# Optimization experiments

Measured on AMD Instinct MI355X. Metric: run time of the kernel, lower is better.

## Reference

```python
import jax, jax.numpy as jnp
import numpy as np

DN = jax.lax.conv_dimension_numbers((1, 32, 32, 32, 1), (3, 3, 3, 1, 32), ('NDHWC', 'DHWIO', 'NDHWC'))


def setup_inputs() -> dict:
    key = jax.random.key(0)
    k0, k1, k2, k3, k4 = jax.random.split(key, 5)
    B = 64
    x = jax.random.normal(k0, (B, 32, 32, 32, 1), dtype=jnp.float32)
    # conv weights in DHWIO layout; kaiming-ish scale
    w1 = jax.random.normal(k1, (3, 3, 3, 1, 32), dtype=jnp.float32) * (1.0 / np.sqrt(27 * 1))
    b1 = jax.random.normal(k2, (32,), dtype=jnp.float32) * 0.01
    w2 = jax.random.normal(k3, (3, 3, 3, 32, 64), dtype=jnp.float32) * (1.0 / np.sqrt(27 * 32))
    b2 = jax.random.normal(k4, (64,), dtype=jnp.float32) * 0.01
    return {"x": x, "w1": w1, "b1": b1, "w2": w2, "b2": b2}


def _conv3d_valid(x, w):
    # x: [B, D, H, W, C_in], w: [kD, kH, kW, C_in, C_out] -> [B, D-2, H-2, W-2, C_out]
    dn = jax.lax.conv_dimension_numbers(x.shape, w.shape, ('NDHWC', 'DHWIO', 'NDHWC'))
    return jax.lax.conv_general_dilated(x, w, window_strides=(1, 1, 1),
                                        padding='VALID', dimension_numbers=dn)


def reference(x, w1, b1, w2, b2):
    # Dense input -> all voxels active, so spconv's gather-GEMM-scatter equals
    # a dense valid 3D conv. ReLU acts on active-site features == dense ReLU.
    h = jax.nn.relu(_conv3d_valid(x, w1) + b1)        # [B, 30, 30, 30, 32]
    h = jax.nn.relu(_conv3d_valid(h, w2) + b2)        # [B, 28, 28, 28, 64]
    # spconv ToDense returns NCDHW
    return jnp.transpose(h, (0, 4, 1, 2, 3))          # [B, 64, 28, 28, 28]
```

## Files before the change

kernel.cpp:

```cpp
#include <hip/hip_runtime.h>
#include <cstdint>
#include <cstddef>

typedef __attribute__((ext_vector_type(8))) short bf16x8;
typedef __attribute__((ext_vector_type(4))) float f32x4;
typedef unsigned short u16;

#define H1_ROW_B   1920
#define H1_BATCH   (30 * 30 * 960)
#define LDS_STRIDE 1952
#define B_LDS_OFF  (36 * LDS_STRIDE)
#define OUT_CSTR   21952

__device__ __forceinline__ u16 f2bf(float f) {
    union { float f; unsigned u; } v; v.f = f;
    unsigned r = v.u + 0x7FFF + ((v.u >> 16) & 1);
    return (u16)(r >> 16);
}

__device__ __forceinline__ void fma4(float4& a, float s, const float4& w) {
    a.x = fmaf(s, w.x, a.x);
    a.y = fmaf(s, w.y, a.y);
    a.z = fmaf(s, w.z, a.z);
    a.w = fmaf(s, w.w, a.w);
}

__global__ __launch_bounds__(256) void conv1_relu(
    const float* __restrict__ x, const float* __restrict__ w1,
    const float* __restrict__ b1, u16* __restrict__ h1, int b0)
{
    __shared__ float wl[27 * 32 + 32];

    const int z   = blockIdx.x;
    const int yt  = blockIdx.y;
    const int bl  = blockIdx.z;
    const int b   = b0 + bl;
    const int tid = threadIdx.x;

    for (int i = tid; i < 27 * 32; i += 256) wl[i] = w1[i];
    if (tid < 32) wl[27 * 32 + tid] = b1[tid];
    __syncthreads();

    const int c4   = tid & 7;
    const int slot = tid >> 3;

    const float4 bias = *reinterpret_cast<const float4*>(&wl[27 * 32 + c4 * 4]);
    const float* xb  = x + (size_t)b * 32768;
    u16*         h1b = h1 + (size_t)bl * H1_BATCH;

    if (slot < 30) {
#pragma unroll 1
        for (int j = 0; j < 3; ++j) {
            const int p  = slot + 30 * j;
            const int yy = p / 15;
            const int xx = (p - yy * 15) * 2;
            const int y  = yt * 6 + yy;

            float4 acc0 = bias, acc1 = bias;
#pragma unroll
            for (int kd = 0; kd < 3; ++kd) {
#pragma unroll
                for (int kh = 0; kh < 3; ++kh) {
                    const float* row = xb + ((size_t)(z + kd) * 32 + (y + kh)) * 32 + xx;
                    const float2 v01 = *reinterpret_cast<const float2*>(row);
                    const float2 v23 = *reinterpret_cast<const float2*>(row + 2);
                    const int t = (kd * 3 + kh) * 3;
                    const float4 w0  = *reinterpret_cast<const float4*>(&wl[(t + 0) * 32 + c4 * 4]);
                    const float4 w1v = *reinterpret_cast<const float4*>(&wl[(t + 1) * 32 + c4 * 4]);
                    const float4 w2v = *reinterpret_cast<const float4*>(&wl[(t + 2) * 32 + c4 * 4]);
                    fma4(acc0, v01.x, w0);
                    fma4(acc0, v01.y, w1v);
                    fma4(acc0, v23.x, w2v);
                    fma4(acc1, v01.y, w0);
                    fma4(acc1, v23.x, w1v);
                    fma4(acc1, v23.y, w2v);
                }
            }
            ushort4 s0, s1;
            s0.x = f2bf(fmaxf(acc0.x, 0.f)); s0.y = f2bf(fmaxf(acc0.y, 0.f));
            s0.z = f2bf(fmaxf(acc0.z, 0.f)); s0.w = f2bf(fmaxf(acc0.w, 0.f));
            s1.x = f2bf(fmaxf(acc1.x, 0.f)); s1.y = f2bf(fmaxf(acc1.y, 0.f));
            s1.z = f2bf(fmaxf(acc1.z, 0.f)); s1.w = f2bf(fmaxf(acc1.w, 0.f));
            u16* dst = h1b + ((size_t)(z * 30 + y) * 30 + xx) * 32 + c4 * 4;
            *reinterpret_cast<ushort4*>(dst)      = s0;
            *reinterpret_cast<ushort4*>(dst + 32) = s1;
        }
    }
}

__global__ __launch_bounds__(256) void pack_w2(
    const float* __restrict__ w2, u16* __restrict__ wB)
{
    const int tap = blockIdx.x;
    const int tid = threadIdx.x;
    const int nt = tid >> 6;
    const int l  = tid & 63;
    const int r = l & 15, q = l >> 4;
    u16* dst = wB + ((size_t)(tap * 4 + nt) * 64 + l) * 8;
#pragma unroll
    for (int j = 0; j < 8; ++j)
        dst[j] = f2bf(w2[(size_t)(tap * 32 + q * 8 + j) * 64 + nt * 16 + r]);
}

template<int NMT, int XOUT>
__device__ __forceinline__ void conv2_body(
    const unsigned char* smem, const char* wBb,
    const float* __restrict__ b2, float* __restrict__ out,
    int b, int y0, int z0, int zw, int wv, int l)
{
    const int r = l & 15, q = l >> 4;
    const int yl = r >> 2, xg = r & 3;

    f32x4 acc[NMT][4];
#pragma unroll
    for (int nt = 0; nt < 4; ++nt) {
        const float bv = b2[nt * 16 + r];
        const f32x4 bi = {bv, bv, bv, bv};
#pragma unroll
        for (int mt = 0; mt < NMT; ++mt) acc[mt][nt] = bi;
    }

    const unsigned char* aBase =
        smem + (zw * 6 + yl) * LDS_STRIDE + (XOUT + xg) * 64 + q * 16;
    const unsigned char* bBase = smem + B_LDS_OFF + (size_t)l * 16;

#pragma unroll
    for (int tap = 0; tap < 27; ++tap) {
        if (tap < 26 && wv == ((tap + 1) & 7)) {
            const char* bsrc = wBb + (size_t)(tap + 1) * 4096 + l * 16;
            unsigned char* bdst = const_cast<unsigned char*>(
                smem) + B_LDS_OFF + ((tap + 1) & 1) * 4096 + l * 16;
#pragma unroll
            for (int k = 0; k < 4; ++k)
                __builtin_amdgcn_global_load_lds(
                    (const __attribute__((address_space(1))) void*)(bsrc + k * 1024),
                    (__attribute__((address_space(3))) void*)(bdst + k * 1024), 16, 0, 0);
        }

        const unsigned char* bb = bBase + (tap & 1) * 4096;
        const bf16x8 B0 = *reinterpret_cast<const bf16x8*>(bb);
        const bf16x8 B1 = *reinterpret_cast<const bf16x8*>(bb + 1024);
        const bf16x8 B2 = *reinterpret_cast<const bf16x8*>(bb + 2048);
        const bf16x8 B3 = *reinterpret_cast<const bf16x8*>(bb + 3072);

        const int kd = tap / 9;
        const int kh = (tap - kd * 9) / 3;
        const int kw = tap - kd * 9 - kh * 3;
        const unsigned char* ap = aBase + (kd * 6 + kh) * LDS_STRIDE + kw * 64;

        __builtin_amdgcn_s_setprio(1);
#pragma unroll
        for (int mt = 0; mt < NMT; ++mt) {
            const bf16x8 a = *reinterpret_cast<const bf16x8*>(ap + mt * 256);
            acc[mt][0] = __builtin_amdgcn_mfma_f32_16x16x32_bf16(a, B0, acc[mt][0], 0, 0, 0);
            acc[mt][1] = __builtin_amdgcn_mfma_f32_16x16x32_bf16(a, B1, acc[mt][1], 0, 0, 0);
            acc[mt][2] = __builtin_amdgcn_mfma_f32_16x16x32_bf16(a, B2, acc[mt][2], 0, 0, 0);
            acc[mt][3] = __builtin_amdgcn_mfma_f32_16x16x32_bf16(a, B3, acc[mt][3], 0, 0, 0);
        }
        __builtin_amdgcn_s_setprio(0);

        __syncthreads();
    }

    const int z = z0 + zw;
    float* ob = out + ((size_t)b * 64 + r) * OUT_CSTR
                    + (size_t)z * 784 + (size_t)(y0 + q) * 28 + XOUT;
#pragma unroll
    for (int mt = 0; mt < NMT; ++mt) {
#pragma unroll
        for (int nt = 0; nt < 4; ++nt) {
            const f32x4 v = acc[mt][nt];
            float4 st;
            st.x = fmaxf(v.x, 0.f);
            st.y = fmaxf(v.y, 0.f);
            st.z = fmaxf(v.z, 0.f);
            st.w = fmaxf(v.w, 0.f);
            *reinterpret_cast<float4*>(ob + (size_t)nt * 16 * OUT_CSTR + mt * 4) = st;
        }
    }
}

__global__ __launch_bounds__(512, 4) void conv2_mfma(
    const u16* __restrict__ h1, const u16* __restrict__ wB,
    const float* __restrict__ b2, float* __restrict__ out, int b0)
{
    __shared__ __align__(16) unsigned char smem[B_LDS_OFF + 8192];

    const int g   = gridDim.x;
    const int bid = blockIdx.x;
    const int lb  = (g % 8 == 0) ? ((bid & 7) * (g >> 3) + (bid >> 3)) : bid;

    const int t0  = lb % 49;
    const int bl  = lb / 49;
    const int yg  = t0 % 7;
    const int zt  = t0 / 7;

    const int b  = b0 + bl;
    const int y0 = yg * 4, z0 = zt * 4;
    const int tid = threadIdx.x;
    const int wv  = tid >> 6;
    const int l   = tid & 63;
    const int zw  = wv >> 1;
    const int xh  = wv & 1;

    const char* wBb = (const char*)wB;

    {
        const char* gbase = (const char*)(h1 + (size_t)bl * H1_BATCH);
        for (int c = wv; c < 72; c += 8) {
            const int rid = c >> 1, half = c & 1;
            const int zz = rid / 6, yy = rid - zz * 6;
            const char* src = gbase
                + (size_t)((z0 + zz) * 30 + (y0 + yy)) * H1_ROW_B
                + half * 896 + l * 16;
            unsigned char* dst = smem + rid * LDS_STRIDE + half * 896 + l * 16;
            __builtin_amdgcn_global_load_lds(
                (const __attribute__((address_space(1))) void*)src,
                (__attribute__((address_space(3))) void*)dst, 16, 0, 0);
        }
    }
    if (wv == 0) {
        const char* bsrc = wBb + l * 16;
        unsigned char* bdst = smem + B_LDS_OFF + l * 16;
#pragma unroll
        for (int k = 0; k < 4; ++k)
            __builtin_amdgcn_global_load_lds(
                (const __attribute__((address_space(1))) void*)(bsrc + k * 1024),
                (__attribute__((address_space(3))) void*)(bdst + k * 1024), 16, 0, 0);
    }
    __syncthreads();

    if (xh == 0)
        conv2_body<4, 0>(smem, wBb, b2, out, b, y0, z0, zw, wv, l);
    else
        conv2_body<3, 16>(smem, wBb, b2, out, b, y0, z0, zw, wv, l);
}

extern "C" void kernel_launch(void* const* d_in, const int* in_sizes, int n_in,
                              void* d_out, int out_size, void* d_ws, size_t ws_size,
                              hipStream_t stream)
{
    const float* x  = (const float*)d_in[0];
    const float* w1 = (const float*)d_in[1];
    const float* b1 = (const float*)d_in[2];
    const float* w2 = (const float*)d_in[3];
    const float* b2 = (const float*)d_in[4];
    float* out = (float*)d_out;

    u16* wB = (u16*)d_ws;
    u16* h1 = (u16*)((char*)d_ws + 131072);

    pack_w2<<<27, 256, 0, stream>>>(w2, wB);

    const size_t per_batch = (size_t)H1_BATCH * 2;
    size_t avail = ws_size > 131072 ? ws_size - 131072 : 0;
    int bchunk = (int)(avail / per_batch);
    if (bchunk < 1)  bchunk = 1;
    if (bchunk > 64) bchunk = 64;

    for (int b0 = 0; b0 < 64; b0 += bchunk) {
        int bc = 64 - b0;
        if (bc > bchunk) bc = bchunk;
        conv1_relu<<<dim3(30, 5, bc), 256, 0, stream>>>(x, w1, b1, h1, b0);
        conv2_mfma<<<dim3(49 * bc), 512, 0, stream>>>(h1, wB, b2, out, b0);
    }
}
```

Baseline: 304.3 us.

## Split conv2 tap loop into two MFMA halves with deeper weight prefetch

Reworks the conv2 inner loop so each tap's MFMAs are split into two halves around a raw s_barrier. The first half of the next tap's B fragments is read into registers early, and the global-to-LDS weight prefetch now runs two taps ahead instead of one. The goal is to hide LDS read and global load latency behind MFMA work and to drop the full __syncthreads, whose implicit waits stall every wave. It adds an extra barrier per tap, manual vmcnt waits and more register pressure, and any ordering mistake in the double buffer could cause a race.

```diff
diff --git a/kernel.cpp b/kernel.cpp
--- a/kernel.cpp
+++ b/kernel.cpp
@@ -23,6 +23,12 @@
     a.y = fmaf(s, w.y, a.y);
     a.z = fmaf(s, w.z, a.z);
     a.w = fmaf(s, w.w, a.w);
+}
+
+__device__ __forceinline__ void gld_lds(const char* src, unsigned char* dst) {
+    __builtin_amdgcn_global_load_lds(
+        (const __attribute__((address_space(1))) void*)src,
+        (__attribute__((address_space(3))) void*)dst, 16, 0, 0);
 }
 
 __global__ __launch_bounds__(256) void conv1_relu(
@@ -124,42 +130,65 @@
         smem + (zw * 6 + yl) * LDS_STRIDE + (XOUT + xg) * 64 + q * 16;
     const unsigned char* bBase = smem + B_LDS_OFF + (size_t)l * 16;
 
+    bf16x8 B01a = *reinterpret_cast<const bf16x8*>(bBase);
+    bf16x8 B01b = *reinterpret_cast<const bf16x8*>(bBase + 1024);
+    bf16x8 A_cur[NMT];
+    bf16x8 B23a, B23b;
+
 #pragma unroll
     for (int tap = 0; tap < 27; ++tap) {
-        if (tap < 26 && wv == ((tap + 1) & 7)) {
-            const char* bsrc = wBb + (size_t)(tap + 1) * 4096 + l * 16;
-            unsigned char* bdst = const_cast<unsigned char*>(
-                smem) + B_LDS_OFF + ((tap + 1) & 1) * 4096 + l * 16;
-#pragma unroll
-            for (int k = 0; k < 4; ++k)
-                __builtin_amdgcn_global_load_lds(
-                    (const __attribute__((address_space(1))) void*)(bsrc + k * 1024),
-                    (__attribute__((address_space(3))) void*)(bdst + k * 1024), 16, 0, 0);
-        }
-
-        const unsigned char* bb = bBase + (tap & 1) * 4096;
-        const bf16x8 B0 = *reinterpret_cast<const bf16x8*>(bb);
-        const bf16x8 B1 = *reinterpret_cast<const bf16x8*>(bb + 1024);
-        const bf16x8 B2 = *reinterpret_cast<const bf16x8*>(bb + 2048);
-        const bf16x8 B3 = *reinterpret_cast<const bf16x8*>(bb + 3072);
-
         const int kd = tap / 9;
         const int kh = (tap - kd * 9) / 3;
         const int kw = tap - kd * 9 - kh * 3;
         const unsigned char* ap = aBase + (kd * 6 + kh) * LDS_STRIDE + kw * 64;
+        const unsigned char* bb = bBase + (tap & 1) * 4096;
+
+#pragma unroll
+        for (int mt = 0; mt < NMT; ++mt)
+            A_cur[mt] = *reinterpret_cast<const bf16x8*>(ap + mt * 256);
+        B23a = *reinterpret_cast<const bf16x8*>(bb + 2048);
+        B23b = *reinterpret_cast<const bf16x8*>(bb + 3072);
 
         __builtin_amdgcn_s_setprio(1);
 #pragma unroll
         for (int mt = 0; mt < NMT; ++mt) {
-            const bf16x8 a = *reinterpret_cast<const bf16x8*>(ap + mt * 256);
-            acc[mt][0] = __builtin_amdgcn_mfma_f32_16x16x32_bf16(a, B0, acc[mt][0], 0, 0, 0);
-            acc[mt][1] = __builtin_amdgcn_mfma_f32_16x16x32_bf16(a, B1, acc[mt][1], 0, 0, 0);
-            acc[mt][2] = __builtin_amdgcn_mfma_f32_16x16x32_bf16(a, B2, acc[mt][2], 0, 0, 0);
-            acc[mt][3] = __builtin_amdgcn_mfma_f32_16x16x32_bf16(a, B3, acc[mt][3], 0, 0, 0);
+            acc[mt][0] = __builtin_amdgcn_mfma_f32_16x16x32_bf16(A_cur[mt], B01a, acc[mt][0], 0, 0, 0);
+            acc[mt][1] = __builtin_amdgcn_mfma_f32_16x16x32_bf16(A_cur[mt], B01b, acc[mt][1], 0, 0, 0);
         }
         __builtin_amdgcn_s_setprio(0);
 
-        __syncthreads();
+        if (tap < 26 && wv == ((tap + 1) & 7))
+            asm volatile("s_waitcnt vmcnt(0)");
+
+        __builtin_amdgcn_sched_barrier(0);
+        __builtin_amdgcn_s_barrier();
+        __builtin_amdgcn_sched_barrier(0);
+
+        if (tap < 26) {
+            const unsigned char* bn = bBase + ((tap + 1) & 1) * 4096;
+            B01a = *reinterpret_cast<const bf16x8*>(bn);
+            B01b = *reinterpret_cast<const bf16x8*>(bn + 1024);
+        }
+        if (tap < 25 && wv == ((tap + 2) & 7)) {
+            const char* bsrc = wBb + (size_t)(tap + 2) * 4096 + l * 16;
+            unsigned char* bdst = const_cast<unsigned char*>(smem)
+                + B_LDS_OFF + ((tap + 2) & 1) * 4096 + l * 16;
+#pragma unroll
+            for (int k = 0; k < 4; ++k)
+                gld_lds(bsrc + k * 1024, bdst + k * 1024);
+        }
+
+        __builtin_amdgcn_s_setprio(1);
+#pragma unroll
+        for (int mt = 0; mt < NMT; ++mt) {
+            acc[mt][2] = __builtin_amdgcn_mfma_f32_16x16x32_bf16(A_cur[mt], B23a, acc[mt][2], 0, 0, 0);
+            acc[mt][3] = __builtin_amdgcn_mfma_f32_16x16x32_bf16(A_cur[mt], B23b, acc[mt][3], 0, 0, 0);
+        }
+        __builtin_amdgcn_s_setprio(0);
+
+        __builtin_amdgcn_sched_barrier(0);
+        __builtin_amdgcn_s_barrier();
+        __builtin_amdgcn_sched_barrier(0);
     }
 
     const int z = z0 + zw;
@@ -214,9 +243,7 @@
                 + (size_t)((z0 + zz) * 30 + (y0 + yy)) * H1_ROW_B
                 + half * 896 + l * 16;
             unsigned char* dst = smem + rid * LDS_STRIDE + half * 896 + l * 16;
-            __builtin_amdgcn_global_load_lds(
-                (const __attribute__((address_space(1))) void*)src,
-                (__attribute__((address_space(3))) void*)dst, 16, 0, 0);
+            gld_lds(src, dst);
         }
     }
     if (wv == 0) {
@@ -224,11 +251,17 @@
         unsigned char* bdst = smem + B_LDS_OFF + l * 16;
 #pragma unroll
         for (int k = 0; k < 4; ++k)
-            __builtin_amdgcn_global_load_lds(
-                (const __attribute__((address_space(1))) void*)(bsrc + k * 1024),
-                (__attribute__((address_space(3))) void*)(bdst + k * 1024), 16, 0, 0);
+            gld_lds(bsrc + k * 1024, bdst + k * 1024);
     }
     __syncthreads();
+
+    if (wv == 1) {
+        const char* bsrc = wBb + 4096 + l * 16;
+        unsigned char* bdst = smem + B_LDS_OFF + 4096 + l * 16;
+#pragma unroll
+        for (int k = 0; k < 4; ++k)
+            gld_lds(bsrc + k * 1024, bdst + k * 1024);
+    }
 
     if (xh == 0)
         conv2_body<4, 0>(smem, wBb, b2, out, b, y0, z0, zw, wv, l);
```

Result: slower. 338.8 us (+11.3%).
